# Kernel tuning notes

Measured on AMD Instinct MI355X. Metric: run time of the kernel, lower is better.

The kernel has to match this reference:

```python
import jax, jax.numpy as jnp
import numpy as np

N, L, K = 2048, 256, 16

def setup_inputs() -> dict:
    rng = np.random.default_rng(0)
    # per level: wavelet index = l (distinct across levels), plus K-1 random distinct rest indices
    sel = np.zeros((L, K), dtype=np.int64)
    wav = np.arange(L, dtype=np.int64)
    all_idx = np.arange(N)
    for l in range(L):
        others = rng.choice(np.delete(all_idx, l), size=K - 1, replace=False)
        sel[l] = np.sort(np.concatenate([[l], others]))
    key = jax.random.key(0)
    k1, k2 = jax.random.split(key)
    M = jax.random.normal(k1, (N, N), dtype=jnp.float32)
    A = 0.5 * (M + M.T)  # symmetric matrix, as MMF expects
    O_all = jax.random.normal(k2, (L, K, K), dtype=jnp.float32) / np.float32(K) ** 0.5
    return {"A": A, "O_all": O_all, "sel_idx": jnp.asarray(sel), "wav_idx": jnp.asarray(wav)}


def reference(A, O_all, sel_idx, wav_idx):
    # Torch builds a dense NxN U = eye with O scattered into the KxK block at
    # sel_idx x sel_idx, then A <- U A U^T and right <- U @ right.
    # Equivalent efficient form: only the K selected rows/cols change.
    n = A.shape[0]

    def step(carry, xs):
        A, right = carry
        O, idx = xs  # O: (K,K), idx: (K,)
        A = A.at[idx].set(O @ A[idx])              # U @ A   : rewrite K rows
        A = A.at[:, idx].set(A[:, idx] @ O.T)      # ... @ U^T: rewrite K cols
        right = right.at[idx].set(O @ right[idx])  # right <- U @ right
        return (A, right), None

    right0 = jnp.eye(n, dtype=A.dtype)
    (A_f, right), _ = jax.lax.scan(step, (A, right0), (O_all, sel_idx))

    # final_active_index: 1 everywhere except wavelet indices
    active = jnp.ones((n,), dtype=A.dtype).at[wav_idx].set(0.0)
    # left_index = eye - diag(diag(outer)) + outer  -> diag all ones, off-diag = a_i*a_j
    left = jnp.outer(active, active)
    left = left.at[jnp.diag_indices(n)].set(1.0)
    D = A_f * left
    A_rec = right.T @ D @ right
    return (A_rec, right, D)
```

## Files before the change

### kernel.cpp

```cpp
#include <hip/hip_runtime.h>

#define N 2048
#define LEV 256
#define KS 16

typedef __attribute__((ext_vector_type(8))) short bfx8;
typedef __attribute__((ext_vector_type(4))) float fx4;
typedef unsigned short u16;
typedef unsigned int u32;

static const size_t NN = (size_t)N * N;

__device__ inline u16 bf16_rne(float f) {
    u32 u = __builtin_bit_cast(u32, f);
    u32 r = (u + 0x7FFFu + ((u >> 16) & 1u)) >> 16;
    return (u16)r;
}
__device__ inline float bf16_f(u16 h) {
    u32 u = ((u32)h) << 16;
    return __builtin_bit_cast(float, u);
}

#define GLDS16(gp, lp) __builtin_amdgcn_global_load_lds( \
    (const __attribute__((address_space(1))) void*)(uintptr_t)(gp), \
    (__attribute__((address_space(3))) void*)(u32)(uintptr_t)(lp), 16, 0, 0)

__device__ inline float qadd(float x) {
#if __has_builtin(__builtin_amdgcn_mov_dpp)
    int a = __builtin_amdgcn_mov_dpp(__builtin_bit_cast(int, x), 0xB1, 0xF, 0xF, true);
    float y = x + __builtin_bit_cast(float, a);
    int b = __builtin_amdgcn_mov_dpp(__builtin_bit_cast(int, y), 0x4E, 0xF, 0xF, true);
    return y + __builtin_bit_cast(float, b);
#else
    float y = x + __shfl_xor(x, 1);
    return y + __shfl_xor(y, 2);
#endif
}

__global__ __launch_bounds__(64)
void front_k(const float* __restrict__ O_all, const int* __restrict__ sel,
             float* __restrict__ RT, u16* __restrict__ rth,
             const float* __restrict__ A, u16* __restrict__ a2h) {
    __shared__ float x[2048];
    const int lane = threadIdx.x;

    if (blockIdx.x >= 2048) {
        u16* a2l = a2h + NN;
        size_t p = (((size_t)blockIdx.x - 2048) * 64 + lane) * 8;
        float4 v0 = *(const float4*)(A + p);
        float4 v1 = *(const float4*)(A + p + 4);
        float vv[8] = {v0.x, v0.y, v0.z, v0.w, v1.x, v1.y, v1.z, v1.w};
        bfx8 hs, ls;
        #pragma unroll
        for (int i = 0; i < 8; ++i) {
            u16 h = bf16_rne(vv[i]);
            hs[i] = (short)h;
            ls[i] = (short)bf16_rne(vv[i] - bf16_f(h));
        }
        *(bfx8*)(a2h + p) = hs;
        *(bfx8*)(a2l + p) = ls;
        return;
    }

    const int i    = lane >> 2;
    const int kg   = lane & 3;
    const int col  = blockIdx.x;

    const float4 z = make_float4(0.f, 0.f, 0.f, 0.f);
    #pragma unroll
    for (int q = 0; q < 8; ++q) *(float4*)&x[q * 256 + lane * 4] = z;
    if (lane == 0) x[col] = 1.0f;

    const float* obase = O_all + i * KS + kg * 4;
    const int*   gbase = sel + kg * 4;

#define CMP(f, g, wv) { \
    float p = f.x * x[g.x] + f.y * x[g.y] + f.z * x[g.z] + f.w * x[g.w]; \
    p = qadd(p); \
    if (kg == 0) x[wv] = p; }

    float4 f0 = *(const float4*)(obase);
    int4   g0 = *(const int4*)(gbase);
    int    w0 = sel[i];
    float4 f1 = *(const float4*)(obase + 256);
    int4   g1 = *(const int4*)(gbase + KS);
    int    w1 = sel[KS + i];

    for (int l = 0; l < LEV; l += 2) {
        float4 f2, f3; int4 g2, g3; int w2, w3;
        if (l + 2 < LEV) {
            f2 = *(const float4*)(obase + (size_t)(l + 2) * 256);
            g2 = *(const int4*)(gbase + (l + 2) * KS);
            w2 = sel[(l + 2) * KS + i];
            f3 = *(const float4*)(obase + (size_t)(l + 3) * 256);
            g3 = *(const int4*)(gbase + (l + 3) * KS);
            w3 = sel[(l + 3) * KS + i];
        } else { f2 = f0; g2 = g0; w2 = w0; f3 = f1; g3 = g1; w3 = w1; }

        CMP(f0, g0, w0)
        CMP(f1, g1, w1)
        f0 = f2; g0 = g2; w0 = w2;
        f1 = f3; g1 = g3; w1 = w3;
    }
#undef CMP

    u16* rtl = rth + NN;
    #pragma unroll
    for (int q = 0; q < 8; ++q) {
        float4 v = *(const float4*)&x[q * 256 + lane * 4];
        *(float4*)&RT[(size_t)col * N + q * 256 + lane * 4] = v;
        float vv[4] = {v.x, v.y, v.z, v.w};
        u16 hh[4], ll[4];
        #pragma unroll
        for (int e = 0; e < 4; ++e) {
            hh[e] = bf16_rne(vv[e]);
            ll[e] = bf16_rne(vv[e] - bf16_f(hh[e]));
        }
        const size_t po = (size_t)col * N + q * 256 + lane * 4;
        *(ushort4*)(rth + po) = make_ushort4(hh[0], hh[1], hh[2], hh[3]);
        *(ushort4*)(rtl + po) = make_ushort4(ll[0], ll[1], ll[2], ll[3]);
    }
}

__global__ __launch_bounds__(256)
void split_rt_k(const float* __restrict__ RT, u16* __restrict__ r2h,
                float* __restrict__ Rrm) {
    __shared__ float t[64][65];
    u16* r2l = r2h + NN;
    const int r0 = (blockIdx.x >> 5) * 64, c0 = (blockIdx.x & 31) * 64;
    #pragma unroll
    for (int i = 0; i < 16; ++i) {
        int q = i * 256 + threadIdx.x;
        int rr = q >> 6, cc = q & 63;
        t[rr][cc] = RT[(size_t)(r0 + rr) * N + c0 + cc];
    }
    __syncthreads();
    #pragma unroll
    for (int i = 0; i < 16; ++i) {
        int q = i * 256 + threadIdx.x;
        int rr = q >> 6, cc = q & 63;
        float w = t[cc][rr];
        u16 h2 = bf16_rne(w);
        size_t pt = (size_t)(c0 + rr) * N + r0 + cc;
        r2h[pt] = h2;
        r2l[pt] = bf16_rne(w - bf16_f(h2));
        Rrm[pt] = w;
    }
}

__global__ __launch_bounds__(256)
void unsplit_k(const u16* __restrict__ hi, float* __restrict__ dst) {
    const u16* lo = hi + NN;
    size_t p = ((size_t)blockIdx.x * 256 + threadIdx.x) * 8;
    bfx8 hs = *(const bfx8*)(hi + p);
    bfx8 ls = *(const bfx8*)(lo + p);
    float4 o0, o1;
    o0.x = bf16_f((u16)hs[0]) + bf16_f((u16)ls[0]);
    o0.y = bf16_f((u16)hs[1]) + bf16_f((u16)ls[1]);
    o0.z = bf16_f((u16)hs[2]) + bf16_f((u16)ls[2]);
    o0.w = bf16_f((u16)hs[3]) + bf16_f((u16)ls[3]);
    o1.x = bf16_f((u16)hs[4]) + bf16_f((u16)ls[4]);
    o1.y = bf16_f((u16)hs[5]) + bf16_f((u16)ls[5]);
    o1.z = bf16_f((u16)hs[6]) + bf16_f((u16)ls[6]);
    o1.w = bf16_f((u16)hs[7]) + bf16_f((u16)ls[7]);
    *(float4*)(dst + p)     = o0;
    *(float4*)(dst + p + 4) = o1;
}

template<int MASKED, int OMODE>
__global__ __launch_bounds__(256)
void gemm_bf3(const u16* __restrict__ Xp, const u16* __restrict__ Yp,
              float* __restrict__ Cf, u16* __restrict__ Cs,
              const int* __restrict__ wav, int Lw) {
    __shared__ __align__(16) u16 sm[24576];
    __shared__ float rowf[128], colf[64];

    const int tid = threadIdx.x;
    const int xcd = blockIdx.x & 7, idx = blockIdx.x >> 3;
    const int sup = 4 * xcd + (idx >> 4);
    const int wi4 = idx & 15;
    const int by = (sup >> 3) * 4 + (wi4 >> 2);
    const int bx = (sup & 7) * 4 + (wi4 & 3);
    const int i0 = by * 128, j0 = bx * 64;
    const int lane = tid & 63, w = tid >> 6;
    const int wm = (w >> 1) * 64, wn = (w & 1) * 32;
    const int fr = lane & 15;

    if (MASKED) {
        if (tid < 128) rowf[tid] = 1.0f;
        if (tid >= 128 && tid < 192) colf[tid - 128] = 1.0f;
        __syncthreads();
        for (int t = tid; t < Lw; t += 256) {
            int wv = wav[t];
            int dr = wv - i0; if (0 <= dr && dr < 128) rowf[dr] = 0.0f;
            int dc = wv - j0; if (0 <= dc && dc < 64)  colf[dc] = 0.0f;
        }
    }

    fx4 acc[4][2];
    #pragma unroll
    for (int m = 0; m < 4; ++m)
        #pragma unroll
        for (int n = 0; n < 2; ++n)
            acc[m][n] = (fx4)0.0f;

    const u16* Xh = Xp; const u16* Xl = Xp + NN;
    const u16* Yh = Yp; const u16* Yl = Yp + NN;

    const int rl   = lane >> 3;
    const int gcol = ((lane & 7) ^ rl) << 3;
    const int wq   = w * 1024;

    #define STAGE(kt) { \
        const int k0s = (kt) * 64; \
        char* lb0 = (char*)sm + wq; \
        _Pragma("unroll") \
        for (int q = 0; q < 4; ++q) { \
            const int row = q * 32 + w * 8 + rl; \
            const size_t xo = (size_t)(i0 + row) * N + k0s + gcol; \
            GLDS16(Xh + xo, lb0 + q * 4096); \
            GLDS16(Xl + xo, lb0 + 16384 + q * 4096); \
        } \
        _Pragma("unroll") \
        for (int q = 0; q < 2; ++q) { \
            const int row = q * 32 + w * 8 + rl; \
            const size_t yo = (size_t)(j0 + row) * N + k0s + gcol; \
            GLDS16(Yh + yo, lb0 + 32768 + q * 4096); \
            GLDS16(Yl + yo, lb0 + 40960 + q * 4096); \
        } }

    const int kq  = (lane >> 4) << 4;
    const int frx = (fr & 7) << 4;

    #define COMPUTE() { \
        const char* base = (const char*)sm; \
        _Pragma("unroll") \
        for (int s = 0; s < 2; ++s) { \
            const int cb = s * 64 + kq; \
            bfx8 ah[4], al[4]; \
            _Pragma("unroll") \
            for (int m = 0; m < 4; ++m) { \
                const int off = (wm + m * 16 + fr) * 128 + (cb ^ frx); \
                ah[m] = *(const bfx8*)(base + off); \
                al[m] = *(const bfx8*)(base + 16384 + off); \
            } \
            _Pragma("unroll") \
            for (int n = 0; n < 2; ++n) { \
                const int off = (wn + n * 16 + fr) * 128 + (cb ^ frx); \
                bfx8 bh = *(const bfx8*)(base + 32768 + off); \
                bfx8 bl = *(const bfx8*)(base + 40960 + off); \
                _Pragma("unroll") \
                for (int m = 0; m < 4; ++m) { \
                    acc[m][n] = __builtin_amdgcn_mfma_f32_16x16x32_bf16(ah[m], bh, acc[m][n], 0, 0, 0); \
                    acc[m][n] = __builtin_amdgcn_mfma_f32_16x16x32_bf16(ah[m], bl, acc[m][n], 0, 0, 0); \
                    acc[m][n] = __builtin_amdgcn_mfma_f32_16x16x32_bf16(al[m], bh, acc[m][n], 0, 0, 0); \
                } \
            } \
        } }

    constexpr int NT = N / 64;
    for (int kt = 0; kt < NT; ++kt) {
        STAGE(kt)
        __syncthreads();
        COMPUTE()
        __syncthreads();
    }

    const int crow0 = (lane >> 4) * 4;
    #pragma unroll
    for (int m = 0; m < 4; ++m) {
        #pragma unroll
        for (int n = 0; n < 2; ++n) {
            #pragma unroll
            for (int r = 0; r < 4; ++r) {
                const int li = wm + m * 16 + crow0 + r;
                const int lj = wn + n * 16 + fr;
                float v = acc[m][n][r];
                if (MASKED) {
                    if (i0 + li != j0 + lj) v *= rowf[li] * colf[lj];
                }
                const size_t off = (size_t)(i0 + li) * N + j0 + lj;
                if (OMODE == 0) {
                    Cf[off] = v;
                } else {
                    u16 h = bf16_rne(v);
                    Cs[off]      = h;
                    Cs[NN + off] = bf16_rne(v - bf16_f(h));
                }
            }
        }
    }
    #undef STAGE
    #undef COMPUTE
}

template<int MASKED, int OMODE>
__global__ __launch_bounds__(256)
void gemm_bf3_s(const u16* __restrict__ Xp, const u16* __restrict__ Yp,
                float* __restrict__ Cf, u16* __restrict__ Cs,
                const int* __restrict__ wav, int Lw) {
    __shared__ __align__(16) u16 sm[16384];
    __shared__ float rowf[64], colf[64];

    const int tid = threadIdx.x;
    const int xcd = blockIdx.x & 7, idx = blockIdx.x >> 3;
    const int sup = 8 * xcd + (idx >> 4);
    const int wi4 = idx & 15;
    const int by = (sup >> 3) * 4 + (wi4 >> 2);
    const int bx = (sup & 7) * 4 + (wi4 & 3);
    const int i0 = by * 64, j0 = bx * 64;
    const int lane = tid & 63, w = tid >> 6;
    const int wm = (w >> 1) * 32, wn = (w & 1) * 32;
    const int fr = lane & 15;

    if (MASKED) {
        if (tid < 64) rowf[tid] = 1.0f;
        if (tid >= 128 && tid < 192) colf[tid - 128] = 1.0f;
        __syncthreads();
        for (int t = tid; t < Lw; t += 256) {
            int wv = wav[t];
            int dr = wv - i0; if (0 <= dr && dr < 64) rowf[dr] = 0.0f;
            int dc = wv - j0; if (0 <= dc && dc < 64) colf[dc] = 0.0f;
        }
    }

    fx4 acc[2][2];
    #pragma unroll
    for (int m = 0; m < 2; ++m)
        #pragma unroll
        for (int n = 0; n < 2; ++n)
            acc[m][n] = (fx4)0.0f;

    const u16* Xh = Xp; const u16* Xl = Xp + NN;
    const u16* Yh = Yp; const u16* Yl = Yp + NN;

    const int rl   = lane >> 3;
    const int gcol = ((lane & 7) ^ rl) << 3;
    const int wq   = w * 1024;
    const int kq   = (lane >> 4) << 4;
    const int frx  = (fr & 7) << 4;

    constexpr int NT = N / 64;
    for (int kt = 0; kt < NT; ++kt) {
        const int k0s = kt * 64;
        {
            char* lb0 = (char*)sm + wq;
            #pragma unroll
            for (int q = 0; q < 2; ++q) {
                const int row = q * 32 + w * 8 + rl;
                const size_t xo = (size_t)(i0 + row) * N + k0s + gcol;
                const size_t yo = (size_t)(j0 + row) * N + k0s + gcol;
                GLDS16(Xh + xo, lb0 + q * 4096);
                GLDS16(Xl + xo, lb0 + 8192 + q * 4096);
                GLDS16(Yh + yo, lb0 + 16384 + q * 4096);
                GLDS16(Yl + yo, lb0 + 24576 + q * 4096);
            }
        }
        __syncthreads();
        {
            const char* base = (const char*)sm;
            #pragma unroll
            for (int s = 0; s < 2; ++s) {
                const int cb = s * 64 + kq;
                bfx8 ah[2], al[2];
                #pragma unroll
                for (int m = 0; m < 2; ++m) {
                    const int off = (wm + m * 16 + fr) * 128 + (cb ^ frx);
                    ah[m] = *(const bfx8*)(base + off);
                    al[m] = *(const bfx8*)(base + 8192 + off);
                }
                #pragma unroll
                for (int n = 0; n < 2; ++n) {
                    const int off = (wn + n * 16 + fr) * 128 + (cb ^ frx);
                    bfx8 bh = *(const bfx8*)(base + 16384 + off);
                    bfx8 bl = *(const bfx8*)(base + 24576 + off);
                    #pragma unroll
                    for (int m = 0; m < 2; ++m) {
                        acc[m][n] = __builtin_amdgcn_mfma_f32_16x16x32_bf16(ah[m], bh, acc[m][n], 0, 0, 0);
                        acc[m][n] = __builtin_amdgcn_mfma_f32_16x16x32_bf16(ah[m], bl, acc[m][n], 0, 0, 0);
                        acc[m][n] = __builtin_amdgcn_mfma_f32_16x16x32_bf16(al[m], bh, acc[m][n], 0, 0, 0);
                    }
                }
            }
        }
        __syncthreads();
    }

    const int crow0 = (lane >> 4) * 4;
    #pragma unroll
    for (int m = 0; m < 2; ++m) {
        #pragma unroll
        for (int n = 0; n < 2; ++n) {
            #pragma unroll
            for (int r = 0; r < 4; ++r) {
                const int li = wm + m * 16 + crow0 + r;
                const int lj = wn + n * 16 + fr;
                float v = acc[m][n][r];
                if (MASKED) {
                    if (i0 + li != j0 + lj) v *= rowf[li] * colf[lj];
                }
                const size_t off = (size_t)(i0 + li) * N + j0 + lj;
                if (OMODE == 0) {
                    Cf[off] = v;
                } else {
                    u16 h = bf16_rne(v);
                    Cs[off]      = h;
                    Cs[NN + off] = bf16_rne(v - bf16_f(h));
                }
            }
        }
    }
}

extern "C" void kernel_launch(void* const* d_in, const int* in_sizes, int n_in,
                              void* d_out, int out_size, void* d_ws, size_t ws_size,
                              hipStream_t stream) {
    const float* A     = (const float*)d_in[0];
    const float* O_all = (const float*)d_in[1];
    const int*   sel   = (const int*)d_in[2];
    const int*   wav   = (const int*)d_in[3];
    const int    Lw    = in_sizes[3];

    float* O1 = (float*)d_out;
    float* O2 = O1 + NN;
    float* O3 = O1 + 2 * NN;

    u16*   W1u = (u16*)d_ws;
    u16*   W2u = (u16*)((char*)d_ws + 2 * NN * sizeof(u16));
    u16*   O1u = (u16*)O1;
    u16*   O3u = (u16*)O3;

    const int SGRID = (int)(NN / (256 * 8));

    front_k<<<2048 + (int)(NN / (64 * 8)), 64, 0, stream>>>(O_all, sel, O3, W1u, A, W2u);
    split_rt_k<<<(N / 64) * (N / 64), 256, 0, stream>>>(O3, O1u, O2);

    gemm_bf3_s<0, 1><<<1024, 256, 0, stream>>>(O1u, W2u, nullptr, O3u, nullptr, 0);
    gemm_bf3<1, 1><<<512, 256, 0, stream>>>(O3u, O1u, nullptr, W2u, wav, Lw);
    gemm_bf3<0, 1><<<512, 256, 0, stream>>>(W1u, W2u, nullptr, O3u, nullptr, 0);
    gemm_bf3<0, 0><<<512, 256, 0, stream>>>(O3u, W1u, O1, nullptr, nullptr, 0);
    unsplit_k<<<SGRID, 256, 0, stream>>>(W2u, O3);
}
```

Measured before the change: 278.0 us.

## Compute only upper-triangular tiles for symmetric GEMMs and mirror-store transposes

The two GEMMs whose outputs are symmetric (the masked A_f-like product and the final reconstruction) now launch only the 528 upper-triangular 64x64 tiles. Each off-diagonal tile is staged through shared memory and also written transposed to the mirrored location. The first GEMM switches from the 1024-block small-tile kernel to the 512-block kernel. This roughly halves MFMA work for those two GEMMs, at the cost of a serial triangular index decode loop, extra LDS staging and uneven per-block store work.

```diff
diff --git a/kernel.cpp b/kernel.cpp
--- a/kernel.cpp
+++ b/kernel.cpp
@@ -296,18 +296,18 @@
 
 template<int MASKED, int OMODE>
 __global__ __launch_bounds__(256)
-void gemm_bf3_s(const u16* __restrict__ Xp, const u16* __restrict__ Yp,
-                float* __restrict__ Cf, u16* __restrict__ Cs,
-                const int* __restrict__ wav, int Lw) {
+void gemm_sym(const u16* __restrict__ Xp, const u16* __restrict__ Yp,
+              float* __restrict__ Cf, u16* __restrict__ Cs,
+              const int* __restrict__ wav, int Lw) {
     __shared__ __align__(16) u16 sm[16384];
     __shared__ float rowf[64], colf[64];
 
     const int tid = threadIdx.x;
-    const int xcd = blockIdx.x & 7, idx = blockIdx.x >> 3;
-    const int sup = 8 * xcd + (idx >> 4);
-    const int wi4 = idx & 15;
-    const int by = (sup >> 3) * 4 + (wi4 >> 2);
-    const int bx = (sup & 7) * 4 + (wi4 & 3);
+    int swz = (blockIdx.x & 7) * 66 + (blockIdx.x >> 3);
+    int t = swz, by = 0;
+    #pragma unroll 1
+    while (t >= 32 - by) { t -= 32 - by; ++by; }
+    const int bx = by + t;
     const int i0 = by * 64, j0 = bx * 64;
     const int lane = tid & 63, w = tid >> 6;
     const int wm = (w >> 1) * 32, wn = (w & 1) * 32;
@@ -317,8 +317,8 @@
         if (tid < 64) rowf[tid] = 1.0f;
         if (tid >= 128 && tid < 192) colf[tid - 128] = 1.0f;
         __syncthreads();
-        for (int t = tid; t < Lw; t += 256) {
-            int wv = wav[t];
+        for (int t2 = tid; t2 < Lw; t2 += 256) {
+            int wv = wav[t2];
             int dr = wv - i0; if (0 <= dr && dr < 64) rowf[dr] = 0.0f;
             int dc = wv - j0; if (0 <= dc && dc < 64) colf[dc] = 0.0f;
         }
@@ -386,6 +386,7 @@
         __syncthreads();
     }
 
+    float* Ct = (float*)sm;
     const int crow0 = (lane >> 4) * 4;
     #pragma unroll
     for (int m = 0; m < 2; ++m) {
@@ -399,6 +400,7 @@
                 if (MASKED) {
                     if (i0 + li != j0 + lj) v *= rowf[li] * colf[lj];
                 }
+                Ct[li * 65 + lj] = v;
                 const size_t off = (size_t)(i0 + li) * N + j0 + lj;
                 if (OMODE == 0) {
                     Cf[off] = v;
@@ -408,6 +410,34 @@
                     Cs[NN + off] = bf16_rne(v - bf16_f(h));
                 }
             }
+        }
+    }
+
+    if (by != bx) {
+        __syncthreads();
+        const int rr  = tid >> 2;
+        const int cc0 = (tid & 3) * 16;
+        float v[16];
+        #pragma unroll
+        for (int e = 0; e < 16; ++e) v[e] = Ct[(cc0 + e) * 65 + rr];
+        const size_t off = (size_t)(j0 + rr) * N + i0 + cc0;
+        if (OMODE == 0) {
+            #pragma unroll
+            for (int q = 0; q < 4; ++q)
+                *(float4*)(Cf + off + q * 4) =
+                    make_float4(v[q*4], v[q*4+1], v[q*4+2], v[q*4+3]);
+        } else {
+            bfx8 hs[2], ls[2];
+            #pragma unroll
+            for (int e = 0; e < 16; ++e) {
+                u16 h = bf16_rne(v[e]);
+                hs[e >> 3][e & 7] = (short)h;
+                ls[e >> 3][e & 7] = (short)bf16_rne(v[e] - bf16_f(h));
+            }
+            *(bfx8*)(Cs + off)          = hs[0];
+            *(bfx8*)(Cs + off + 8)      = hs[1];
+            *(bfx8*)(Cs + NN + off)     = ls[0];
+            *(bfx8*)(Cs + NN + off + 8) = ls[1];
         }
     }
 }
@@ -435,9 +465,9 @@
     front_k<<<2048 + (int)(NN / (64 * 8)), 64, 0, stream>>>(O_all, sel, O3, W1u, A, W2u);
     split_rt_k<<<(N / 64) * (N / 64), 256, 0, stream>>>(O3, O1u, O2);
 
-    gemm_bf3_s<0, 1><<<1024, 256, 0, stream>>>(O1u, W2u, nullptr, O3u, nullptr, 0);
-    gemm_bf3<1, 1><<<512, 256, 0, stream>>>(O3u, O1u, nullptr, W2u, wav, Lw);
+    gemm_bf3<0, 1><<<512, 256, 0, stream>>>(O1u, W2u, nullptr, O3u, nullptr, 0);
+    gemm_sym<1, 1><<<528, 256, 0, stream>>>(O3u, O1u, nullptr, W2u, wav, Lw);
     gemm_bf3<0, 1><<<512, 256, 0, stream>>>(W1u, W2u, nullptr, O3u, nullptr, 0);
-    gemm_bf3<0, 0><<<512, 256, 0, stream>>>(O3u, W1u, O1, nullptr, nullptr, 0);
+    gemm_sym<0, 0><<<528, 256, 0, stream>>>(O3u, W1u, O1, nullptr, nullptr, 0);
     unsplit_k<<<SGRID, 256, 0, stream>>>(W2u, O3);
 }
```

Measured after the change: 243.5 us. 12.4% less time.
